# Kernel optimization log

Hardware: AMD Instinct MI355X
Metric: run time of the kernel (lower is better)

## Reference

```python
import jax, jax.numpy as jnp
import numpy as np

D_CHAR, D_HID, LEN_VOC = 256, 1024, 512
BSZ, MAX_LEN = 128, 256


def setup_inputs() -> dict:
    key = jax.random.key(0)
    ks = jax.random.split(key, 14)
    s = 1.0 / np.sqrt(D_HID)  # PyTorch RNN/Linear init scale
    u = lambda k, shape: jax.random.uniform(k, shape, jnp.float32, -s, s)
    return {
        "inputs": jax.random.randint(ks[0], (BSZ, MAX_LEN), 0, LEN_VOC),
        "outputs": jax.random.randint(ks[1], (BSZ, MAX_LEN), 0, LEN_VOC),
        "emb": jax.random.normal(ks[2], (LEN_VOC, D_CHAR), jnp.float32),
        "enc_Wih": u(ks[3], (D_HID, D_CHAR)),
        "enc_Whh": u(ks[4], (D_HID, D_HID)),
        "enc_bih": u(ks[5], (D_HID,)),
        "enc_bhh": u(ks[6], (D_HID,)),
        "dec_Wih": u(ks[7], (D_HID, D_CHAR)),
        "dec_Whh": u(ks[8], (D_HID, D_HID)),
        "dec_bih": u(ks[9], (D_HID,)),
        "dec_bhh": u(ks[10], (D_HID,)),
        "out_W": u(ks[11], (LEN_VOC, D_HID)),
        "out_b": u(ks[12], (LEN_VOC,)),
    }


def rnn_scan(x_seq, h0, Wih, Whh, bih, bhh):
    """Elman RNN (tanh), batch_first input [B, T, D] -> (h_T [B,H], all h [T,B,H]).
    h_t = tanh(W_ih x_t + b_ih + W_hh h_{t-1} + b_hh), matching torch.nn.RNN."""
    # Precompute input projection for all timesteps (one big GEMM).
    xp = jnp.einsum('btd,hd->bth', x_seq, Wih) + bih + bhh  # [B,T,H]
    xp = jnp.swapaxes(xp, 0, 1)  # [T,B,H] for scan

    def step(h, x):
        h = jnp.tanh(x + h @ Whh.T)
        return h, h

    hT, hs = jax.lax.scan(step, h0, xp)
    return hT, hs


def reference(inputs, outputs, emb, enc_Wih, enc_Whh, enc_bih, enc_bhh,
              dec_Wih, dec_Whh, dec_bih, dec_bhh, out_W, out_b):
    bsz, max_len = inputs.shape
    # Encoder over input char embeddings, zero initial hidden.
    embs = emb[inputs]  # [B,T,Dc]
    h0 = jnp.zeros((bsz, D_HID), jnp.float32)
    hT, _ = rnn_scan(embs, h0, enc_Wih, enc_Whh, enc_bih, enc_bhh)
    # Teacher-forced decoder: step 0 gets zero input, step t gets emb(outputs[:, t-1]).
    dec_in = jnp.concatenate(
        [jnp.zeros((bsz, 1, D_CHAR), jnp.float32), emb[outputs[:, :-1]]], axis=1)
    _, dec_hs = rnn_scan(dec_in, hT, dec_Wih, dec_Whh, dec_bih, dec_bhh)  # [T,B,H]
    # decoder_states.transpose(0,1).view(-1, d_hid)
    states = jnp.swapaxes(dec_hs, 0, 1).reshape(-1, D_HID)  # [B*T, H]
    logits = states @ out_W.T + out_b  # [B*T, V]
    return jax.nn.log_softmax(logits, axis=1)
```

## Files before the change

### kernel.cpp

```cpp
#include <hip/hip_runtime.h>


typedef short short8 __attribute__((ext_vector_type(8)));
typedef float floatx4 __attribute__((ext_vector_type(4)));

#define WS_WIN    0ull
#define WS_STATES (2ull << 20)
#define WS_WB     (66ull << 20)

#define HS_STRIDE 1032

__device__ __forceinline__ float bf2f(unsigned short u) {
  union { unsigned u; float f; } x; x.u = ((unsigned)u) << 16; return x.f;
}
__device__ __forceinline__ unsigned short f2bf(float f) {
  union { float f; unsigned u; } x; x.f = f;
  unsigned r = x.u + 0x7FFFu + ((x.u >> 16) & 1u);
  return (unsigned short)(r >> 16);
}
__device__ __forceinline__ unsigned pkminu16(unsigned a, unsigned b) {
  unsigned d;
  asm("v_pk_min_u16 %0, %1, %2" : "=v"(d) : "v"(a), "v"(b));
  return d;
}

__global__ __launch_bounds__(256) void cvt_kernel(
    const float* __restrict__ src, unsigned short* __restrict__ dst, int n)
{
  const int i = (blockIdx.x * 256 + threadIdx.x) * 4;
  if (i >= n) return;
  const float4 v = *(const float4*)(src + i);
  unsigned short o[4] = {f2bf(v.x), f2bf(v.y), f2bf(v.z), f2bf(v.w)};
  *(uint2*)(dst + i) = *(const uint2*)o;
}

__global__ __launch_bounds__(256) void gemm_bt_kernel(
    const unsigned short* __restrict__ Abase,
    const int mode,
    const unsigned short* __restrict__ Bmat,
    const float* __restrict__ bias0,
    const float* __restrict__ bias1,
    unsigned short* __restrict__ outp_bf,
    float* __restrict__ outp_f,
    const int K, const int N, const int nbn)
{
  __shared__ unsigned short As[64][264];
  __shared__ unsigned short Bs[64][264];
  __shared__ const unsigned short* rowsrc[64];

  const int tid = threadIdx.x;
  const int lane = tid & 63;
  const int wave = tid >> 6;
  const int bn = blockIdx.x % nbn;
  const int bm = blockIdx.x / nbn;
  const int m0 = bm * 64;
  const int j0 = bn * 64;

  if (tid < 64) {
    const int m = m0 + tid;
    const unsigned short* src;
    if (mode == 0) {
      src = Abase + (size_t)m * K;
    } else {
      src = Abase + ((size_t)(m & 255) * 128 + (m >> 8)) * 1024;
    }
    rowsrc[tid] = src;
  }

  const floatx4 zf = {0.f, 0.f, 0.f, 0.f};
  floatx4 acc0 = zf, acc1 = zf, acc2 = zf, acc3 = zf;

  for (int kc = 0; kc < K; kc += 256) {
    __syncthreads();
#pragma unroll
    for (int i = 0; i < 8; ++i) {
      const int idx = i * 256 + tid;
      const int r = idx >> 5;
      const int c = idx & 31;
      const unsigned short* s = rowsrc[r];
      *(short8*)&As[r][c * 8] = *(const short8*)(s + kc + c * 8);
      *(short8*)&Bs[r][c * 8] =
          *(const short8*)(Bmat + (size_t)(j0 + r) * K + kc + c * 8);
    }
    __syncthreads();
    const int ar = 16 * wave + (lane & 15);
    const int kq = (lane >> 4) * 8;
#pragma unroll
    for (int kk = 0; kk < 8; ++kk) {
      const short8 a = *(const short8*)&As[ar][kk * 32 + kq];
      const short8 bv0 = *(const short8*)&Bs[(lane & 15)][kk * 32 + kq];
      acc0 = __builtin_amdgcn_mfma_f32_16x16x32_bf16(a, bv0, acc0, 0, 0, 0);
      const short8 bv1 = *(const short8*)&Bs[16 + (lane & 15)][kk * 32 + kq];
      acc1 = __builtin_amdgcn_mfma_f32_16x16x32_bf16(a, bv1, acc1, 0, 0, 0);
      const short8 bv2 = *(const short8*)&Bs[32 + (lane & 15)][kk * 32 + kq];
      acc2 = __builtin_amdgcn_mfma_f32_16x16x32_bf16(a, bv2, acc2, 0, 0, 0);
      const short8 bv3 = *(const short8*)&Bs[48 + (lane & 15)][kk * 32 + kq];
      acc3 = __builtin_amdgcn_mfma_f32_16x16x32_bf16(a, bv3, acc3, 0, 0, 0);
    }
  }

  float bs[4] = {0.f, 0.f, 0.f, 0.f};
  if (bias0) {
#pragma unroll
    for (int nt = 0; nt < 4; ++nt) {
      const int jj = j0 + nt * 16 + (lane & 15);
      bs[nt] = bias0[jj] + bias1[jj];
    }
  }
  __syncthreads();
  const int rbase = 16 * wave + (lane >> 4) * 4;
  const int cl = lane & 15;

  if (outp_bf) {
#pragma unroll
    for (int i = 0; i < 4; ++i) {
      As[rbase + i][cl]      = f2bf(acc0[i] + bs[0]);
      As[rbase + i][16 + cl] = f2bf(acc1[i] + bs[1]);
      As[rbase + i][32 + cl] = f2bf(acc2[i] + bs[2]);
      As[rbase + i][48 + cl] = f2bf(acc3[i] + bs[3]);
    }
    __syncthreads();
#pragma unroll
    for (int i = 0; i < 2; ++i) {
      const int idx = i * 256 + tid;
      const int r = idx >> 3;
      const int c = idx & 7;
      *(short8*)(outp_bf + (size_t)(m0 + r) * N + j0 + c * 8) =
          *(const short8*)&As[r][c * 8];
    }
  } else {
    float (*Asf)[66] = (float(*)[66]) & As[0][0];
#pragma unroll
    for (int i = 0; i < 4; ++i) {
      Asf[rbase + i][cl]      = acc0[i] + bs[0];
      Asf[rbase + i][16 + cl] = acc1[i] + bs[1];
      Asf[rbase + i][32 + cl] = acc2[i] + bs[2];
      Asf[rbase + i][48 + cl] = acc3[i] + bs[3];
    }
    __syncthreads();
#pragma unroll
    for (int i = 0; i < 4; ++i) {
      const int idx = i * 256 + tid;
      const int r = idx >> 4;
      const int c = idx & 15;
      *(float4*)(outp_f + (size_t)(m0 + r) * N + j0 + c * 4) =
          *(const float4*)&Asf[r][c * 4];
    }
  }
}

__global__ __launch_bounds__(256) void rnn_scan5_kernel(
    const unsigned short* __restrict__ WhhE,
    const unsigned short* __restrict__ WhhD,
    const unsigned short* __restrict__ projE,
    const unsigned short* __restrict__ projD,
    const float* __restrict__ decBih,
    const float* __restrict__ decBhh,
    const int* __restrict__ intoks,
    const int* __restrict__ outtoks,
    unsigned short* __restrict__ win,
    unsigned short* __restrict__ states)
{
  __shared__ unsigned short hs[2 * 16 * HS_STRIDE];
  __shared__ int toks[16 * 257];

  const int tid = threadIdx.x;
  const int lane = tid & 63;
  const int wave = tid >> 6;
  const int g = blockIdx.x & 7;
  const int slot = blockIdx.x >> 3;
  const int b0 = g * 16;
  const int q = lane >> 4;
  const int cl = lane & 15;
  const int jwb = slot * 64 + wave * 16;
  const int jq4 = jwb + q * 4;
  const bool own = (((tid & 127) >> 3) == slot);
  const size_t prodoff = (size_t)(b0 + cl) * 1024 + jq4;

  short8 w[32];
  const floatx4 zf = {0.f, 0.f, 0.f, 0.f};
  unsigned long long obp = 0;

  for (int phase = 0; phase < 2; ++phase) {
    const unsigned short* Whh = phase ? WhhD : WhhE;
    const unsigned short* proj = phase ? projD : projE;
    const int* gt = phase ? outtoks : intoks;
    {
      const unsigned short* wp = Whh + (size_t)(jwb + cl) * 1024 + q * 8;
#pragma unroll
      for (int kk = 0; kk < 32; ++kk) w[kk] = *(const short8*)(wp + kk * 32);
    }
    float xb[4] = {0.f, 0.f, 0.f, 0.f};
    if (phase) {
#pragma unroll
      for (int i = 0; i < 4; ++i) xb[i] = decBih[jq4 + i] + decBhh[jq4 + i];
    }
    __syncthreads();
#pragma unroll
    for (int i = 0; i < 16; ++i) {
      const int idx = i * 256 + tid;
      toks[(idx >> 8) * 257 + (idx & 255)] =
          gt[(size_t)(b0 + (idx >> 8)) * 256 + (idx & 255)];
    }
    __syncthreads();

    for (int t = 0; t < 256; ++t) {
      const int s = phase * 256 + t;
      float xpf[4];
      {
        const int tt = phase ? (t > 0 ? t - 1 : 0) : t;
        const int tok = toks[cl * 257 + tt];
        const uint2 xr = *(const uint2*)(proj + (size_t)tok * 1024 + jq4);
        const unsigned short* xs = (const unsigned short*)&xr;
#pragma unroll
        for (int i = 0; i < 4; ++i) xpf[i] = bf2f(xs[i]);
        if (phase && t == 0) {
#pragma unroll
          for (int i = 0; i < 4; ++i) xpf[i] = xb[i];
        }
      }

      unsigned short* hsb = hs + (s & 1) * (16 * HS_STRIDE);
      if (s > 0) {
        const unsigned short* hprev =
            win + (size_t)((s - 1) & 7) * 131072 + b0 * 1024;
        if (!own) {
          short8 tmp[8];
          for (;;) {
#pragma unroll
            for (int c = 0; c < 8; ++c) {
              const unsigned long long* p =
                  (const unsigned long long*)(hprev + (c * 256 + tid) * 8);
              union { unsigned long long u[2]; short8 s8; } v;
              v.u[0] = __hip_atomic_load(p, __ATOMIC_RELAXED,
                                         __HIP_MEMORY_SCOPE_AGENT);
              v.u[1] = __hip_atomic_load(p + 1, __ATOMIC_RELAXED,
                                         __HIP_MEMORY_SCOPE_AGENT);
              tmp[c] = v.s8;
            }
            const unsigned* du = (const unsigned*)tmp;
            unsigned m0v = 0xFFFFFFFFu, m1v = 0xFFFFFFFFu;
            unsigned m2v = 0xFFFFFFFFu, m3v = 0xFFFFFFFFu;
#pragma unroll
            for (int i = 0; i < 8; ++i) {
              m0v = pkminu16(m0v, du[4 * i + 0] ^ 0xAAAAAAAAu);
              m1v = pkminu16(m1v, du[4 * i + 1] ^ 0xAAAAAAAAu);
              m2v = pkminu16(m2v, du[4 * i + 2] ^ 0xAAAAAAAAu);
              m3v = pkminu16(m3v, du[4 * i + 3] ^ 0xAAAAAAAAu);
            }
            const unsigned mm = pkminu16(pkminu16(m0v, m1v), pkminu16(m2v, m3v));
            const unsigned hz = (mm - 0x00010001u) & ~mm & 0x80008000u;
            if (hz == 0u) {
#pragma unroll
              for (int c = 0; c < 8; ++c) {
                const int gg = c * 256 + tid;
                *(short8*)&hsb[(gg >> 7) * HS_STRIDE + (gg & 127) * 8] = tmp[c];
              }
              break;
            }
            __builtin_amdgcn_s_sleep(1);
          }
        }
        *(unsigned long long*)&hsb[cl * HS_STRIDE + jq4] = obp;
      }
      __builtin_amdgcn_sched_barrier(0);
      asm volatile("s_waitcnt lgkmcnt(0)" ::: "memory");
      __builtin_amdgcn_s_barrier();
      __builtin_amdgcn_sched_barrier(0);

      floatx4 acc0 = zf, acc1 = zf, acc2 = zf, acc3 = zf;
      if (s > 0) {
        const unsigned short* hrow = &hsb[cl * HS_STRIDE + q * 8];
#pragma unroll
        for (int kk = 0; kk < 32; kk += 4) {
          const short8 a0 = *(const short8*)(hrow + (kk + 0) * 32);
          const short8 a1 = *(const short8*)(hrow + (kk + 1) * 32);
          const short8 a2 = *(const short8*)(hrow + (kk + 2) * 32);
          const short8 a3 = *(const short8*)(hrow + (kk + 3) * 32);
          acc0 = __builtin_amdgcn_mfma_f32_16x16x32_bf16(w[kk + 0], a0, acc0, 0, 0, 0);
          acc1 = __builtin_amdgcn_mfma_f32_16x16x32_bf16(w[kk + 1], a1, acc1, 0, 0, 0);
          acc2 = __builtin_amdgcn_mfma_f32_16x16x32_bf16(w[kk + 2], a2, acc2, 0, 0, 0);
          acc3 = __builtin_amdgcn_mfma_f32_16x16x32_bf16(w[kk + 3], a3, acc3, 0, 0, 0);
        }
      }
      unsigned short ob[4];
#pragma unroll
      for (int i = 0; i < 4; ++i) {
        const float pre = acc0[i] + acc1[i] + acc2[i] + acc3[i] + xpf[i];
        const float e = __expf(2.f * pre);
        ob[i] = f2bf(1.f - 2.f / (e + 1.f));
        if (ob[i] == 0xAAAAu) ob[i] = 0xAAABu;
      }
      obp = *(const unsigned long long*)ob;
      __hip_atomic_store(
          (unsigned long long*)(win + (size_t)(s & 7) * 131072 + prodoff),
          obp, __ATOMIC_RELAXED, __HIP_MEMORY_SCOPE_AGENT);
      if (phase) {
        __builtin_nontemporal_store(
            obp, (unsigned long long*)(states + (size_t)t * 131072 + prodoff));
      }
      if (s >= 2) {
        __hip_atomic_store(
            (unsigned long long*)(win + (size_t)((s - 2) & 7) * 131072 + prodoff),
            0xAAAAAAAAAAAAAAAAull, __ATOMIC_RELAXED, __HIP_MEMORY_SCOPE_AGENT);
      }
    }
  }
}

__global__ __launch_bounds__(256) void logsoftmax_kernel(
    float* __restrict__ logits, const float* __restrict__ outb)
{
  const int row = blockIdx.x * 4 + (threadIdx.x >> 6);
  const int lane = threadIdx.x & 63;
  float* rp = logits + (size_t)row * 512 + lane * 8;
  const float4 a0 = *(const float4*)rp;
  const float4 a1 = *(const float4*)(rp + 4);
  const float4 b0 = *(const float4*)(outb + lane * 8);
  const float4 b1 = *(const float4*)(outb + lane * 8 + 4);
  float v[8] = {a0.x + b0.x, a0.y + b0.y, a0.z + b0.z, a0.w + b0.w,
                a1.x + b1.x, a1.y + b1.y, a1.z + b1.z, a1.w + b1.w};
  float mx = v[0];
#pragma unroll
  for (int i = 1; i < 8; ++i) mx = fmaxf(mx, v[i]);
#pragma unroll
  for (int m = 1; m < 64; m <<= 1) mx = fmaxf(mx, __shfl_xor(mx, m, 64));
  float sum = 0.f;
#pragma unroll
  for (int i = 0; i < 8; ++i) sum += __expf(v[i] - mx);
#pragma unroll
  for (int m = 1; m < 64; m <<= 1) sum += __shfl_xor(sum, m, 64);
  const float lse = mx + __logf(sum);
  float4 o0 = {v[0] - lse, v[1] - lse, v[2] - lse, v[3] - lse};
  float4 o1 = {v[4] - lse, v[5] - lse, v[6] - lse, v[7] - lse};
  *(float4*)rp = o0;
  *(float4*)(rp + 4) = o1;
}

extern "C" void kernel_launch(void* const* d_in, const int* in_sizes, int n_in,
                              void* d_out, int out_size, void* d_ws, size_t ws_size,
                              hipStream_t stream)
{
  const int* inputs  = (const int*)d_in[0];
  const int* outputs = (const int*)d_in[1];
  const float* emb    = (const float*)d_in[2];
  const float* encWih = (const float*)d_in[3];
  const float* encWhh = (const float*)d_in[4];
  const float* encBih = (const float*)d_in[5];
  const float* encBhh = (const float*)d_in[6];
  const float* decWih = (const float*)d_in[7];
  const float* decWhh = (const float*)d_in[8];
  const float* decBih = (const float*)d_in[9];
  const float* decBhh = (const float*)d_in[10];
  const float* outW   = (const float*)d_in[11];
  const float* outB   = (const float*)d_in[12];

  char* ws = (char*)d_ws;
  unsigned short* win    = (unsigned short*)(ws + WS_WIN);
  unsigned short* states = (unsigned short*)(ws + WS_STATES);
  char* wb = ws + WS_WB;
  unsigned short* embB  = (unsigned short*)(wb + 0);
  unsigned short* eWihB = (unsigned short*)(wb + (512ull << 10));
  unsigned short* dWihB = (unsigned short*)(wb + (1ull << 20));
  unsigned short* eWhhB = (unsigned short*)(wb + (2ull << 20));
  unsigned short* dWhhB = (unsigned short*)(wb + (4ull << 20));
  unsigned short* outWB = (unsigned short*)(wb + (6ull << 20));
  unsigned short* projE = (unsigned short*)(wb + (7ull << 20));
  unsigned short* projD = (unsigned short*)(wb + (8ull << 20));
  float* logits = (float*)d_out;

  cvt_kernel<<<128, 256, 0, stream>>>(emb, embB, 512 * 256);
  cvt_kernel<<<256, 256, 0, stream>>>(encWih, eWihB, 1024 * 256);
  cvt_kernel<<<256, 256, 0, stream>>>(decWih, dWihB, 1024 * 256);
  cvt_kernel<<<1024, 256, 0, stream>>>(encWhh, eWhhB, 1024 * 1024);
  cvt_kernel<<<1024, 256, 0, stream>>>(decWhh, dWhhB, 1024 * 1024);
  cvt_kernel<<<512, 256, 0, stream>>>(outW, outWB, 512 * 1024);

  gemm_bt_kernel<<<128, 256, 0, stream>>>(embB, 0, eWihB, encBih, encBhh,
                                          projE, nullptr, 256, 1024, 16);
  gemm_bt_kernel<<<128, 256, 0, stream>>>(embB, 0, dWihB, decBih, decBhh,
                                          projD, nullptr, 256, 1024, 16);

  rnn_scan5_kernel<<<128, 256, 0, stream>>>(eWhhB, dWhhB, projE, projD,
                                            decBih, decBhh, inputs, outputs,
                                            win, states);

  gemm_bt_kernel<<<4096, 256, 0, stream>>>(states, 3, outWB, nullptr, nullptr,
                                           nullptr, logits, 1024, 512, 8);
  logsoftmax_kernel<<<8192, 256, 0, stream>>>(logits, outB);
}
```

Before: 2.029 ms.

## Use 64 wider RNN scan blocks with contiguous cache-bypassing hidden-state polling

The recurrent scan kernel now runs as 64 blocks of 512 threads instead of 128 blocks of 256, so each block owns 128 hidden columns. That halves the number of blocks exchanging hidden state each step. The cross-block poll is rewritten: each thread issues four contiguous 16-byte loads with sc0 sc1 cache-bypass bits in inline asm, checks the sentinel, and only then writes to LDS. The fewer, larger blocks are meant to cut inter-block synchronization traffic, at the cost of more per-block work and register pressure under the 512-thread launch bound.

```diff
diff --git a/kernel.cpp b/kernel.cpp
--- a/kernel.cpp
+++ b/kernel.cpp
@@ -3,6 +3,7 @@
 
 typedef short short8 __attribute__((ext_vector_type(8)));
 typedef float floatx4 __attribute__((ext_vector_type(4)));
+typedef unsigned int uint4v __attribute__((ext_vector_type(4)));
 
 #define WS_WIN    0ull
 #define WS_STATES (2ull << 20)
@@ -149,7 +150,7 @@
   }
 }
 
-__global__ __launch_bounds__(256) void rnn_scan5_kernel(
+__global__ __launch_bounds__(512) void rnn_scan6_kernel(
     const unsigned short* __restrict__ WhhE,
     const unsigned short* __restrict__ WhhD,
     const unsigned short* __restrict__ projE,
@@ -172,14 +173,17 @@
   const int b0 = g * 16;
   const int q = lane >> 4;
   const int cl = lane & 15;
-  const int jwb = slot * 64 + wave * 16;
+  const int jwb = slot * 128 + wave * 16;
   const int jq4 = jwb + q * 4;
-  const bool own = (((tid & 127) >> 3) == slot);
-  const size_t prodoff = (size_t)(b0 + cl) * 1024 + jq4;
+  const int prow = tid >> 5;
+  const int pcc = tid & 31;
+  const int pc32 = pcc * 32;
+  const bool own = ((pcc >> 2) == slot);
 
   short8 w[32];
   const floatx4 zf = {0.f, 0.f, 0.f, 0.f};
   unsigned long long obp = 0;
+  const size_t prodoff = (size_t)(b0 + cl) * 1024 + jq4;
 
   for (int phase = 0; phase < 2; ++phase) {
     const unsigned short* Whh = phase ? WhhD : WhhE;
@@ -197,8 +201,8 @@
     }
     __syncthreads();
 #pragma unroll
-    for (int i = 0; i < 16; ++i) {
-      const int idx = i * 256 + tid;
+    for (int i = 0; i < 8; ++i) {
+      const int idx = i * 512 + tid;
       toks[(idx >> 8) * 257 + (idx & 255)] =
           gt[(size_t)(b0 + (idx >> 8)) * 256 + (idx & 255)];
     }
@@ -225,41 +229,38 @@
         const unsigned short* hprev =
             win + (size_t)((s - 1) & 7) * 131072 + b0 * 1024;
         if (!own) {
-          short8 tmp[8];
+          const unsigned long long paddr =
+              (unsigned long long)(hprev + prow * 1024 + pc32);
+          uint4v d0, d1, d2, d3;
           for (;;) {
-#pragma unroll
-            for (int c = 0; c < 8; ++c) {
-              const unsigned long long* p =
-                  (const unsigned long long*)(hprev + (c * 256 + tid) * 8);
-              union { unsigned long long u[2]; short8 s8; } v;
-              v.u[0] = __hip_atomic_load(p, __ATOMIC_RELAXED,
-                                         __HIP_MEMORY_SCOPE_AGENT);
-              v.u[1] = __hip_atomic_load(p + 1, __ATOMIC_RELAXED,
-                                         __HIP_MEMORY_SCOPE_AGENT);
-              tmp[c] = v.s8;
-            }
-            const unsigned* du = (const unsigned*)tmp;
+            asm volatile(
+                "global_load_dwordx4 %0, %4, off sc0 sc1\n\t"
+                "global_load_dwordx4 %1, %4, off offset:16 sc0 sc1\n\t"
+                "global_load_dwordx4 %2, %4, off offset:32 sc0 sc1\n\t"
+                "global_load_dwordx4 %3, %4, off offset:48 sc0 sc1\n\t"
+                "s_waitcnt vmcnt(0)"
+                : "=&v"(d0), "=&v"(d1), "=&v"(d2), "=&v"(d3)
+                : "v"(paddr)
+                : "memory");
             unsigned m0v = 0xFFFFFFFFu, m1v = 0xFFFFFFFFu;
             unsigned m2v = 0xFFFFFFFFu, m3v = 0xFFFFFFFFu;
 #pragma unroll
-            for (int i = 0; i < 8; ++i) {
-              m0v = pkminu16(m0v, du[4 * i + 0] ^ 0xAAAAAAAAu);
-              m1v = pkminu16(m1v, du[4 * i + 1] ^ 0xAAAAAAAAu);
-              m2v = pkminu16(m2v, du[4 * i + 2] ^ 0xAAAAAAAAu);
-              m3v = pkminu16(m3v, du[4 * i + 3] ^ 0xAAAAAAAAu);
+            for (int i = 0; i < 4; ++i) {
+              m0v = pkminu16(m0v, d0[i] ^ 0xAAAAAAAAu);
+              m1v = pkminu16(m1v, d1[i] ^ 0xAAAAAAAAu);
+              m2v = pkminu16(m2v, d2[i] ^ 0xAAAAAAAAu);
+              m3v = pkminu16(m3v, d3[i] ^ 0xAAAAAAAAu);
             }
             const unsigned mm = pkminu16(pkminu16(m0v, m1v), pkminu16(m2v, m3v));
             const unsigned hz = (mm - 0x00010001u) & ~mm & 0x80008000u;
-            if (hz == 0u) {
-#pragma unroll
-              for (int c = 0; c < 8; ++c) {
-                const int gg = c * 256 + tid;
-                *(short8*)&hsb[(gg >> 7) * HS_STRIDE + (gg & 127) * 8] = tmp[c];
-              }
-              break;
-            }
+            if (hz == 0u) break;
             __builtin_amdgcn_s_sleep(1);
           }
+          unsigned short* dst = &hsb[prow * HS_STRIDE + pc32];
+          *(uint4v*)(dst + 0)  = d0;
+          *(uint4v*)(dst + 8)  = d1;
+          *(uint4v*)(dst + 16) = d2;
+          *(uint4v*)(dst + 24) = d3;
         }
         *(unsigned long long*)&hsb[cl * HS_STRIDE + jq4] = obp;
       }
@@ -381,9 +382,9 @@
   gemm_bt_kernel<<<128, 256, 0, stream>>>(embB, 0, dWihB, decBih, decBhh,
                                           projD, nullptr, 256, 1024, 16);
 
-  rnn_scan5_kernel<<<128, 256, 0, stream>>>(eWhhB, dWhhB, projE, projD,
-                                            decBih, decBhh, inputs, outputs,
-                                            win, states);
+  rnn_scan6_kernel<<<64, 512, 0, stream>>>(eWhhB, dWhhB, projE, projD,
+                                           decBih, decBhh, inputs, outputs,
+                                           win, states);
 
   gemm_bt_kernel<<<4096, 256, 0, stream>>>(states, 3, outWB, nullptr, nullptr,
                                            nullptr, logits, 1024, 512, 8);
```

Result: faster. 1.830 ms (-9.8%).

## Replace sentinel-poisoned window polling with per-wave step flags and double-buffered hidden state

Applied to the files above, without the earlier changes.

The recurrent scan used to poll the whole previous hidden-state window until no element held a poison value, then reset old entries with the sentinel. Now each wave publishes a per-step counter flag after its hidden-state store. Consumers spin on 64 flags with a ballot, then bulk-load the double-buffered state with cache-bypassing loads. This removes the repeated full-window reloads, the packed-min scans and the extra poison stores, and the compute section runs at raised wave priority. The risk is ordering: correctness relies on the vmcnt wait before the flag store being enough for cross-CU visibility, and the two-slot buffer assumes no block runs more than one step ahead.

```diff
diff --git a/kernel.cpp b/kernel.cpp
--- a/kernel.cpp
+++ b/kernel.cpp
@@ -3,8 +3,9 @@
 
 typedef short short8 __attribute__((ext_vector_type(8)));
 typedef float floatx4 __attribute__((ext_vector_type(4)));
-
-#define WS_WIN    0ull
+typedef unsigned int uint4v __attribute__((ext_vector_type(4)));
+
+#define WS_HBUF   0ull
 #define WS_STATES (2ull << 20)
 #define WS_WB     (66ull << 20)
 
@@ -17,11 +18,6 @@
   union { float f; unsigned u; } x; x.f = f;
   unsigned r = x.u + 0x7FFFu + ((x.u >> 16) & 1u);
   return (unsigned short)(r >> 16);
-}
-__device__ __forceinline__ unsigned pkminu16(unsigned a, unsigned b) {
-  unsigned d;
-  asm("v_pk_min_u16 %0, %1, %2" : "=v"(d) : "v"(a), "v"(b));
-  return d;
 }
 
 __global__ __launch_bounds__(256) void cvt_kernel(
@@ -149,7 +145,7 @@
   }
 }
 
-__global__ __launch_bounds__(256) void rnn_scan5_kernel(
+__global__ __launch_bounds__(256) void rnn_scan8_kernel(
     const unsigned short* __restrict__ WhhE,
     const unsigned short* __restrict__ WhhD,
     const unsigned short* __restrict__ projE,
@@ -158,8 +154,9 @@
     const float* __restrict__ decBhh,
     const int* __restrict__ intoks,
     const int* __restrict__ outtoks,
-    unsigned short* __restrict__ win,
-    unsigned short* __restrict__ states)
+    unsigned short* __restrict__ hbuf,
+    unsigned short* __restrict__ states,
+    unsigned int* __restrict__ flags)
 {
   __shared__ unsigned short hs[2 * 16 * HS_STRIDE];
   __shared__ int toks[16 * 257];
@@ -174,12 +171,12 @@
   const int cl = lane & 15;
   const int jwb = slot * 64 + wave * 16;
   const int jq4 = jwb + q * 4;
-  const bool own = (((tid & 127) >> 3) == slot);
-  const size_t prodoff = (size_t)(b0 + cl) * 1024 + jq4;
+  unsigned int* grpflags = flags + (size_t)g * 1024;
+  const int myflag = (slot * 4 + wave) * 16;
 
   short8 w[32];
   const floatx4 zf = {0.f, 0.f, 0.f, 0.f};
-  unsigned long long obp = 0;
+  const size_t prodoff = (size_t)(b0 + cl) * 1024 + jq4;
 
   for (int phase = 0; phase < 2; ++phase) {
     const unsigned short* Whh = phase ? WhhD : WhhE;
@@ -222,51 +219,51 @@
 
       unsigned short* hsb = hs + (s & 1) * (16 * HS_STRIDE);
       if (s > 0) {
-        const unsigned short* hprev =
-            win + (size_t)((s - 1) & 7) * 131072 + b0 * 1024;
-        if (!own) {
-          short8 tmp[8];
-          for (;;) {
-#pragma unroll
-            for (int c = 0; c < 8; ++c) {
-              const unsigned long long* p =
-                  (const unsigned long long*)(hprev + (c * 256 + tid) * 8);
-              union { unsigned long long u[2]; short8 s8; } v;
-              v.u[0] = __hip_atomic_load(p, __ATOMIC_RELAXED,
-                                         __HIP_MEMORY_SCOPE_AGENT);
-              v.u[1] = __hip_atomic_load(p + 1, __ATOMIC_RELAXED,
-                                         __HIP_MEMORY_SCOPE_AGENT);
-              tmp[c] = v.s8;
-            }
-            const unsigned* du = (const unsigned*)tmp;
-            unsigned m0v = 0xFFFFFFFFu, m1v = 0xFFFFFFFFu;
-            unsigned m2v = 0xFFFFFFFFu, m3v = 0xFFFFFFFFu;
-#pragma unroll
-            for (int i = 0; i < 8; ++i) {
-              m0v = pkminu16(m0v, du[4 * i + 0] ^ 0xAAAAAAAAu);
-              m1v = pkminu16(m1v, du[4 * i + 1] ^ 0xAAAAAAAAu);
-              m2v = pkminu16(m2v, du[4 * i + 2] ^ 0xAAAAAAAAu);
-              m3v = pkminu16(m3v, du[4 * i + 3] ^ 0xAAAAAAAAu);
-            }
-            const unsigned mm = pkminu16(pkminu16(m0v, m1v), pkminu16(m2v, m3v));
-            const unsigned hz = (mm - 0x00010001u) & ~mm & 0x80008000u;
-            if (hz == 0u) {
-#pragma unroll
-              for (int c = 0; c < 8; ++c) {
-                const int gg = c * 256 + tid;
-                *(short8*)&hsb[(gg >> 7) * HS_STRIDE + (gg & 127) * 8] = tmp[c];
-              }
-              break;
-            }
-            __builtin_amdgcn_s_sleep(1);
+        const unsigned target = (unsigned)s;
+        for (;;) {
+          const unsigned f = __hip_atomic_load(&grpflags[lane * 16],
+                                               __ATOMIC_RELAXED,
+                                               __HIP_MEMORY_SCOPE_AGENT);
+          if (__ballot(f < target) == 0ull) break;
+          __builtin_amdgcn_s_sleep(1);
+        }
+        const unsigned short* hrb = hbuf + (size_t)(s & 1) * 131072 + b0 * 1024;
+        uint4v p0, p1, p2, p3, p4, p5, p6, p7;
+        {
+          const unsigned long long a0 = (unsigned long long)(hrb + tid * 8);
+          asm volatile(
+              "global_load_dwordx4 %0, %8, off sc0 sc1\n\t"
+              "global_load_dwordx4 %1, %9, off sc0 sc1\n\t"
+              "global_load_dwordx4 %2, %10, off sc0 sc1\n\t"
+              "global_load_dwordx4 %3, %11, off sc0 sc1\n\t"
+              "global_load_dwordx4 %4, %12, off sc0 sc1\n\t"
+              "global_load_dwordx4 %5, %13, off sc0 sc1\n\t"
+              "global_load_dwordx4 %6, %14, off sc0 sc1\n\t"
+              "global_load_dwordx4 %7, %15, off sc0 sc1\n\t"
+              "s_waitcnt vmcnt(0)"
+              : "=&v"(p0), "=&v"(p1), "=&v"(p2), "=&v"(p3),
+                "=&v"(p4), "=&v"(p5), "=&v"(p6), "=&v"(p7)
+              : "v"(a0),            "v"(a0 + 1 * 4096),
+                "v"(a0 + 2 * 4096), "v"(a0 + 3 * 4096),
+                "v"(a0 + 4 * 4096), "v"(a0 + 5 * 4096),
+                "v"(a0 + 6 * 4096), "v"(a0 + 7 * 4096)
+              : "memory");
+        }
+        __builtin_amdgcn_sched_barrier(0);
+        {
+          uint4v pp[8] = {p0, p1, p2, p3, p4, p5, p6, p7};
+#pragma unroll
+          for (int c = 0; c < 8; ++c) {
+            const int gg = c * 256 + tid;
+            *(uint4v*)&hsb[(gg >> 7) * HS_STRIDE + (gg & 127) * 8] = pp[c];
           }
         }
-        *(unsigned long long*)&hsb[cl * HS_STRIDE + jq4] = obp;
       }
       __builtin_amdgcn_sched_barrier(0);
       asm volatile("s_waitcnt lgkmcnt(0)" ::: "memory");
       __builtin_amdgcn_s_barrier();
       __builtin_amdgcn_sched_barrier(0);
+      __builtin_amdgcn_s_setprio(1);
 
       floatx4 acc0 = zf, acc1 = zf, acc2 = zf, acc3 = zf;
       if (s > 0) {
@@ -289,20 +286,19 @@
         const float pre = acc0[i] + acc1[i] + acc2[i] + acc3[i] + xpf[i];
         const float e = __expf(2.f * pre);
         ob[i] = f2bf(1.f - 2.f / (e + 1.f));
-        if (ob[i] == 0xAAAAu) ob[i] = 0xAAABu;
-      }
-      obp = *(const unsigned long long*)ob;
+      }
+      const unsigned long long obp = *(const unsigned long long*)ob;
       __hip_atomic_store(
-          (unsigned long long*)(win + (size_t)(s & 7) * 131072 + prodoff),
+          (unsigned long long*)(hbuf + (size_t)((s + 1) & 1) * 131072 + prodoff),
           obp, __ATOMIC_RELAXED, __HIP_MEMORY_SCOPE_AGENT);
+      asm volatile("s_waitcnt vmcnt(0)" ::: "memory");
+      if (lane == 0)
+        __hip_atomic_store(&grpflags[myflag], (unsigned)(s + 1),
+                           __ATOMIC_RELAXED, __HIP_MEMORY_SCOPE_AGENT);
+      __builtin_amdgcn_s_setprio(0);
       if (phase) {
         __builtin_nontemporal_store(
             obp, (unsigned long long*)(states + (size_t)t * 131072 + prodoff));
-      }
-      if (s >= 2) {
-        __hip_atomic_store(
-            (unsigned long long*)(win + (size_t)((s - 2) & 7) * 131072 + prodoff),
-            0xAAAAAAAAAAAAAAAAull, __ATOMIC_RELAXED, __HIP_MEMORY_SCOPE_AGENT);
       }
     }
   }
@@ -356,7 +352,7 @@
   const float* outB   = (const float*)d_in[12];
 
   char* ws = (char*)d_ws;
-  unsigned short* win    = (unsigned short*)(ws + WS_WIN);
+  unsigned short* hbuf   = (unsigned short*)(ws + WS_HBUF);
   unsigned short* states = (unsigned short*)(ws + WS_STATES);
   char* wb = ws + WS_WB;
   unsigned short* embB  = (unsigned short*)(wb + 0);
@@ -367,7 +363,10 @@
   unsigned short* outWB = (unsigned short*)(wb + (6ull << 20));
   unsigned short* projE = (unsigned short*)(wb + (7ull << 20));
   unsigned short* projD = (unsigned short*)(wb + (8ull << 20));
+  unsigned int*   flags = (unsigned int*)  (wb + (9ull << 20));
   float* logits = (float*)d_out;
+
+  hipMemsetAsync(flags, 0, 8 * 1024 * sizeof(unsigned int), stream);
 
   cvt_kernel<<<128, 256, 0, stream>>>(emb, embB, 512 * 256);
   cvt_kernel<<<256, 256, 0, stream>>>(encWih, eWihB, 1024 * 256);
@@ -381,9 +380,9 @@
   gemm_bt_kernel<<<128, 256, 0, stream>>>(embB, 0, dWihB, decBih, decBhh,
                                           projD, nullptr, 256, 1024, 16);
 
-  rnn_scan5_kernel<<<128, 256, 0, stream>>>(eWhhB, dWhhB, projE, projD,
+  rnn_scan8_kernel<<<128, 256, 0, stream>>>(eWhhB, dWhhB, projE, projD,
                                             decBih, decBhh, inputs, outputs,
-                                            win, states);
+                                            hbuf, states, flags);
 
   gemm_bt_kernel<<<4096, 256, 0, stream>>>(states, 3, outWB, nullptr, nullptr,
                                            nullptr, logits, 1024, 512, 8);
```

Measured after the change: 1.624 ms. 20.0% less time.
